# Performance work log

Hardware: AMD Instinct MI355X
Metric: run time of the kernel (lower is better)

The kernel has to match this reference:

```python
import jax, jax.numpy as jnp
import numpy as np

T, B, F = 160, 640, 40
HID, PROJ, LAYERS = 768, 256, 3


def lstm_proj_layer(x, Wk, b, Wp, reverse=False):
    # x: [T, B, in]; Wk: [in+PROJ, 4*HID]; b: [4*HID]; Wp: [HID, PROJ]
    nb = x.shape[1]
    c0 = jnp.zeros((nb, HID), x.dtype)
    h0 = jnp.zeros((nb, PROJ), x.dtype)

    def step(carry, xt):
        c, h = carry
        z = jnp.concatenate([xt, h], axis=-1) @ Wk + b
        i, j, f, o = jnp.split(z, 4, axis=-1)  # TF LSTMCell gate order i,j,f,o
        c = jax.nn.sigmoid(f + 1.0) * c + jax.nn.sigmoid(i) * jnp.tanh(j)  # forget_bias=1.0
        h = (jax.nn.sigmoid(o) * jnp.tanh(c)) @ Wp  # projection
        return (c, h), h

    _, ys = jax.lax.scan(step, (c0, h0), x, reverse=reverse)
    return ys  # [T, B, PROJ], time-aligned with input even when reverse=True


def _run_stack(x, params, reverse):
    for (Wk, b, Wp) in params:
        x = lstm_proj_layer(x, Wk, b, Wp, reverse=reverse)
    return x


def setup_inputs() -> dict:
    key = jax.random.key(0)
    keys = jax.random.split(key, 1 + 6 * LAYERS)
    inp = {"batch": jax.random.normal(keys[0], (T, B, F), dtype=jnp.float32)}
    ki = 1
    for d in ("fw", "bw"):
        for l in range(LAYERS):
            in_dim = F if l == 0 else PROJ
            inp[f"Wk_{d}{l}"] = jax.random.normal(keys[ki], (in_dim + PROJ, 4 * HID), dtype=jnp.float32) * 0.05
            inp[f"b_{d}{l}"] = jnp.zeros((4 * HID,), dtype=jnp.float32)
            inp[f"Wp_{d}{l}"] = jax.random.normal(keys[ki + 1], (HID, PROJ), dtype=jnp.float32) * 0.05
            ki += 2
    return inp


def reference(batch,
              Wk_fw0, b_fw0, Wp_fw0, Wk_fw1, b_fw1, Wp_fw1, Wk_fw2, b_fw2, Wp_fw2,
              Wk_bw0, b_bw0, Wp_bw0, Wk_bw1, b_bw1, Wp_bw1, Wk_bw2, b_bw2, Wp_bw2):
    fw_params = [(Wk_fw0, b_fw0, Wp_fw0), (Wk_fw1, b_fw1, Wp_fw1), (Wk_fw2, b_fw2, Wp_fw2)]
    bw_params = [(Wk_bw0, b_bw0, Wp_bw0), (Wk_bw1, b_bw1, Wp_bw1), (Wk_bw2, b_bw2, Wp_bw2)]
    out_fw = _run_stack(batch, fw_params, reverse=False)
    out_bw = _run_stack(batch, bw_params, reverse=True)
    outputs = jnp.concatenate([out_fw, out_bw], axis=2)  # [T, B, 2*PROJ]
    embedded = (outputs[0] + outputs[-1]) / 2.0
    # tf.nn.l2_normalize semantics
    embedded = embedded * jax.lax.rsqrt(jnp.maximum(jnp.sum(embedded * embedded, axis=-1, keepdims=True), 1e-12))
    return embedded
```

## Files before the change

### kernel.cpp

```cpp
#include <hip/hip_runtime.h>


typedef _Float16 h8 __attribute__((ext_vector_type(8)));
typedef float f4 __attribute__((ext_vector_type(4)));

#define T_STEPS 160
#define NB 640
#define HID 768
#define PROJ 256
#define NGATE 3072

__device__ __forceinline__ float sigm(float x) { return 1.0f / (1.0f + __expf(-x)); }
__device__ __forceinline__ float tanh_fast(float x) { return 2.0f / (1.0f + __expf(-2.0f * x)) - 1.0f; }

struct GateArgs {
  const _Float16* A0[6];
  const _Float16* A1[6];
  const _Float16* Bw[6];
  const float*    bias[6];
  float*          cst[6];
  _Float16*       g[6];
  int w0[6];
  int lda0[6];
  int K[6];
  int act[6];
};

struct ProjArgs {
  const _Float16* G[6];
  const _Float16* Wp[6];
  _Float16* out[6];
  _Float16* out2[6];
  int act[6];
};

__global__ __launch_bounds__(256, 3) void gate_step(GateArgs args) {
  const int z = blockIdx.z;
  if (!args.act[z]) return;

  __shared__ __align__(16) char sm[36864];
  _Float16 (*As)[72] = (_Float16(*)[72])sm;
  _Float16 (*Bs)[72] = (_Float16(*)[72])(sm + 18432);
  float (*zs)[65] = (float(*)[65])sm;

  const _Float16* A0 = args.A0[z];
  const _Float16* A1 = args.A1[z];
  const _Float16* Bw = args.Bw[z];
  const int w0 = args.w0[z], lda0 = args.lda0[z], K = args.K[z];
  const int n0 = blockIdx.x * 128;
  const int m0 = blockIdx.y * 128;
  const int tid = threadIdx.x;
  const int lane = tid & 63;
  const int wv = tid >> 6;
  const int wm = (wv & 1) * 64;
  const int wn = (wv >> 1) * 64;

  f4 acc[4][4] = {};

  const int lr = tid >> 3;
  const int lkg = (tid & 7) * 8;

  for (int k0 = 0; k0 < K; k0 += 64) {
    const int gk = k0 + lkg;
    h8 av[4], bv[4];
    if (gk < w0) {
#pragma unroll
      for (int r = 0; r < 4; ++r)
        av[r] = *(const h8*)(A0 + (size_t)(m0 + lr + 32 * r) * lda0 + gk);
    } else {
#pragma unroll
      for (int r = 0; r < 4; ++r)
        av[r] = *(const h8*)(A1 + (size_t)(m0 + lr + 32 * r) * 256 + (gk - w0));
    }
#pragma unroll
    for (int r = 0; r < 4; ++r)
      bv[r] = *(const h8*)(Bw + (size_t)(n0 + lr + 32 * r) * K + gk);
    __syncthreads();
#pragma unroll
    for (int r = 0; r < 4; ++r) {
      *(h8*)&As[lr + 32 * r][lkg] = av[r];
      *(h8*)&Bs[lr + 32 * r][lkg] = bv[r];
    }
    __syncthreads();
#pragma unroll
    for (int kk = 0; kk < 2; ++kk) {
      const int kq = ((lane >> 4) * 8) + kk * 32;
      h8 bf[4];
#pragma unroll
      for (int j = 0; j < 4; ++j)
        bf[j] = *(const h8*)&Bs[wn + (lane & 15) + 16 * j][kq];
#pragma unroll
      for (int i = 0; i < 4; ++i) {
        h8 af = *(const h8*)&As[wm + (lane & 15) + 16 * i][kq];
#pragma unroll
        for (int j = 0; j < 4; ++j)
          acc[i][j] = __builtin_amdgcn_mfma_f32_16x16x32_f16(af, bf[j], acc[i][j], 0, 0, 0);
      }
    }
  }

  const float* bias = args.bias[z];
  float* cstate = args.cst[z];
  _Float16* gout = args.g[z];
#pragma unroll
  for (int p = 0; p < 2; ++p) {
    __syncthreads();
    if ((wv >> 1) == p) {
#pragma unroll
      for (int mi = 0; mi < 4; ++mi)
#pragma unroll
        for (int ni = 0; ni < 4; ++ni)
#pragma unroll
          for (int r = 0; r < 4; ++r) {
            int row = wm + mi * 16 + ((lane >> 4) << 2) + r;
            int col = ni * 16 + (lane & 15);
            zs[row][col] = acc[mi][ni][r];
          }
    }
    __syncthreads();
    const int u0 = (n0 + p * 64) >> 2;
#pragma unroll
    for (int it = 0; it < 8; ++it) {
      int item = it * 256 + tid;
      int row = item >> 4;
      int u = item & 15;
      float zi = zs[row][4 * u + 0] + bias[0 * HID + u0 + u];
      float zj = zs[row][4 * u + 1] + bias[1 * HID + u0 + u];
      float zf = zs[row][4 * u + 2] + bias[2 * HID + u0 + u];
      float zo = zs[row][4 * u + 3] + bias[3 * HID + u0 + u];
      size_t co = (size_t)(m0 + row) * HID + u0 + u;
      float cold = cstate[co];
      float cnew = sigm(zf + 1.0f) * cold + sigm(zi) * tanh_fast(zj);
      float g = sigm(zo) * tanh_fast(cnew);
      cstate[co] = cnew;
      gout[co] = (_Float16)g;
    }
  }
}

__global__ __launch_bounds__(256) void proj_step(ProjArgs args) {
  const int z = blockIdx.z;
  if (!args.act[z]) return;

  __shared__ __align__(16) _Float16 As[64][72];
  __shared__ __align__(16) _Float16 Bs[64][72];

  const _Float16* A = args.G[z];
  const _Float16* B = args.Wp[z];
  const int n0 = blockIdx.x * 64;
  const int m0 = blockIdx.y * 64;
  const int tid = threadIdx.x;
  const int lane = tid & 63;
  const int wv = tid >> 6;
  const int wm = (wv & 1) * 32;
  const int wn = (wv >> 1) * 32;

  f4 acc[2][2] = {};
  const int lr = tid >> 3;
  const int lkg = (tid & 7) * 8;

  for (int k0 = 0; k0 < HID; k0 += 64) {
    const int gk = k0 + lkg;
    h8 av0 = *(const h8*)(A + (size_t)(m0 + lr) * HID + gk);
    h8 av1 = *(const h8*)(A + (size_t)(m0 + lr + 32) * HID + gk);
    h8 bv0 = *(const h8*)(B + (size_t)(n0 + lr) * HID + gk);
    h8 bv1 = *(const h8*)(B + (size_t)(n0 + lr + 32) * HID + gk);
    __syncthreads();
    *(h8*)&As[lr][lkg] = av0;
    *(h8*)&As[lr + 32][lkg] = av1;
    *(h8*)&Bs[lr][lkg] = bv0;
    *(h8*)&Bs[lr + 32][lkg] = bv1;
    __syncthreads();
    const int mr = wm + (lane & 15);
    const int nr = wn + (lane & 15);
#pragma unroll
    for (int kk = 0; kk < 2; ++kk) {
      const int kq = ((lane >> 4) * 8) + kk * 32;
      h8 a0 = *(const h8*)&As[mr][kq];
      h8 a1 = *(const h8*)&As[mr + 16][kq];
      h8 b0 = *(const h8*)&Bs[nr][kq];
      h8 b1 = *(const h8*)&Bs[nr + 16][kq];
      acc[0][0] = __builtin_amdgcn_mfma_f32_16x16x32_f16(a0, b0, acc[0][0], 0, 0, 0);
      acc[0][1] = __builtin_amdgcn_mfma_f32_16x16x32_f16(a0, b1, acc[0][1], 0, 0, 0);
      acc[1][0] = __builtin_amdgcn_mfma_f32_16x16x32_f16(a1, b0, acc[1][0], 0, 0, 0);
      acc[1][1] = __builtin_amdgcn_mfma_f32_16x16x32_f16(a1, b1, acc[1][1], 0, 0, 0);
    }
  }

  _Float16* outp = args.out[z];
  _Float16* out2 = args.out2[z];
#pragma unroll
  for (int mi = 0; mi < 2; ++mi)
#pragma unroll
    for (int ni = 0; ni < 2; ++ni)
#pragma unroll
      for (int r = 0; r < 4; ++r) {
        int row = wm + mi * 16 + ((lane >> 4) << 2) + r;
        int col = wn + ni * 16 + (lane & 15);
        _Float16 v = (_Float16)acc[mi][ni][r];
        size_t o = (size_t)(m0 + row) * PROJ + (n0 + col);
        outp[o] = v;
        if (out2) out2[o] = v;
      }
}

__global__ void convX(const float* __restrict__ X, _Float16* __restrict__ X16, size_t total) {
  size_t i = (size_t)blockIdx.x * 256 + threadIdx.x;
  if (i >= total) return;
  int p = (int)(i & 63);
  size_t tb = i >> 6;
  float v = (p < 40) ? X[tb * 40 + p] : 0.0f;
  X16[i] = (_Float16)v;
}

__global__ void conv_wk(const float* __restrict__ Wk, _Float16* __restrict__ out,
                        int mode, int Kpad, size_t total) {
  size_t i = (size_t)blockIdx.x * 256 + threadIdx.x;
  if (i >= total) return;
  int k = (int)(i % Kpad);
  int n = (int)(i / Kpad);
  int u = n >> 2, g = n & 3;
  int col = g * HID + u;
  float v;
  if (mode == 0) {
    if (k < 40)      v = Wk[(size_t)k * NGATE + col];
    else if (k < 64) v = 0.0f;
    else             v = Wk[(size_t)(k - 24) * NGATE + col];
  } else {
    v = Wk[(size_t)k * NGATE + col];
  }
  out[i] = (_Float16)v;
}

__global__ void conv_wp(const float* __restrict__ Wp, _Float16* __restrict__ out, size_t total) {
  size_t i = (size_t)blockIdx.x * 256 + threadIdx.x;
  if (i >= total) return;
  int k = (int)(i % HID);
  int c = (int)(i / HID);
  out[i] = (_Float16)Wp[(size_t)k * PROJ + c];
}

__global__ __launch_bounds__(256) void readout(const _Float16* __restrict__ E, float* __restrict__ out) {
  const size_t SL = (size_t)NB * PROJ;
  int b = blockIdx.x, tid = threadIdx.x;
  float v[2];
  float ss = 0.0f;
#pragma unroll
  for (int i = 0; i < 2; ++i) {
    int j = tid + i * 256;
    int d = j >> 8, c = j & 255;
    const _Float16* base = E + (size_t)d * 2 * SL;
    float a = (float)base[(size_t)b * PROJ + c];
    float zv = (float)base[SL + (size_t)b * PROJ + c];
    v[i] = 0.5f * (a + zv);
    ss += v[i] * v[i];
  }
#pragma unroll
  for (int off = 32; off; off >>= 1) ss += __shfl_down(ss, off);
  __shared__ float ps[4];
  if ((tid & 63) == 0) ps[tid >> 6] = ss;
  __syncthreads();
  float tot = ps[0] + ps[1] + ps[2] + ps[3];
  float nrm = rsqrtf(fmaxf(tot, 1e-12f));
  out[(size_t)b * 512 + tid] = v[0] * nrm;
  out[(size_t)b * 512 + tid + 256] = v[1] * nrm;
}

extern "C" void kernel_launch(void* const* d_in, const int* in_sizes, int n_in,
                              void* d_out, int out_size, void* d_ws, size_t ws_size,
                              hipStream_t stream) {
  (void)in_sizes; (void)n_in; (void)out_size; (void)ws_size;
  const float* X = (const float*)d_in[0];
  const float* Wk[2][3]; const float* Bi[2][3]; const float* Wp[2][3];
  for (int d = 0; d < 2; ++d)
    for (int l = 0; l < 3; ++l) {
      int base = 1 + d * 9 + l * 3;
      Wk[d][l] = (const float*)d_in[base];
      Bi[d][l] = (const float*)d_in[base + 1];
      Wp[d][l] = (const float*)d_in[base + 2];
    }

  char* ws = (char*)d_ws;
  size_t off = 0;
  auto alloc = [&](size_t bytes) -> void* {
    void* p = ws + off;
    off += (bytes + 255) & ~(size_t)255;
    return p;
  };

  const size_t SL = (size_t)NB * PROJ;

  _Float16* X16 = (_Float16*)alloc((size_t)T_STEPS * NB * 64 * 2);
  _Float16* WkT[2][3];
  for (int d = 0; d < 2; ++d)
    for (int l = 0; l < 3; ++l)
      WkT[d][l] = (_Float16*)alloc((size_t)NGATE * (l == 0 ? 320 : 512) * 2);
  _Float16* WpT[2][3];
  for (int d = 0; d < 2; ++d)
    for (int l = 0; l < 3; ++l)
      WpT[d][l] = (_Float16*)alloc((size_t)PROJ * HID * 2);
  _Float16* Hbuf = (_Float16*)alloc(6UL * 4 * SL * 2);
  float* cst = (float*)alloc(6UL * NB * HID * 4);
  _Float16* gbuf = (_Float16*)alloc(6UL * NB * HID * 2);
  _Float16* embed = (_Float16*)alloc(4UL * SL * 2);

  auto Hslot = [&](int l, int d, int slot) -> _Float16* {
    return Hbuf + (((size_t)(l * 2 + d) * 4) + slot) * SL;
  };

  {
    size_t tot = (size_t)T_STEPS * NB * 64;
    convX<<<dim3((unsigned)((tot + 255) / 256)), 256, 0, stream>>>(X, X16, tot);
  }
  for (int d = 0; d < 2; ++d)
    for (int l = 0; l < 3; ++l) {
      int Kpad = (l == 0) ? 320 : 512;
      size_t tot = (size_t)NGATE * Kpad;
      conv_wk<<<dim3((unsigned)((tot + 255) / 256)), 256, 0, stream>>>(
          Wk[d][l], WkT[d][l], (l == 0) ? 0 : 1, Kpad, tot);
      size_t totp = (size_t)PROJ * HID;
      conv_wp<<<dim3((unsigned)((totp + 255) / 256)), 256, 0, stream>>>(Wp[d][l], WpT[d][l], totp);
    }
  hipMemsetAsync(Hbuf, 0, 6UL * 4 * SL * 2, stream);
  hipMemsetAsync(cst, 0, 6UL * NB * HID * 4, stream);

  for (int s = 0; s <= 161; ++s) {
    GateArgs ga{};
    ProjArgs pa{};
    for (int l = 0; l < 3; ++l)
      for (int d = 0; d < 2; ++d) {
        int z = l * 2 + d;
        int t = s - l;
        if (t < 0 || t > 159) { ga.act[z] = 0; pa.act[z] = 0; continue; }
        int tt = (d == 0) ? t : 159 - t;
        ga.act[z] = 1; pa.act[z] = 1;
        if (l == 0) {
          ga.A0[z] = X16 + (size_t)tt * NB * 64;
          ga.w0[z] = 64; ga.lda0[z] = 64; ga.K[z] = 320;
        } else {
          ga.A0[z] = Hslot(l - 1, d, (tt + 1) & 3);
          ga.w0[z] = 256; ga.lda0[z] = 256; ga.K[z] = 512;
        }
        int rdslot = (d == 0) ? (tt & 3) : ((tt + 2) & 3);
        ga.A1[z] = Hslot(l, d, rdslot);
        ga.Bw[z] = WkT[d][l];
        ga.bias[z] = Bi[d][l];
        ga.cst[z] = cst + (size_t)z * NB * HID;
        ga.g[z] = gbuf + (size_t)z * NB * HID;

        pa.G[z] = gbuf + (size_t)z * NB * HID;
        pa.Wp[z] = WpT[d][l];
        pa.out[z] = Hslot(l, d, (tt + 1) & 3);
        pa.out2[z] = nullptr;
        if (l == 2 && (tt == 0 || tt == 159))
          pa.out2[z] = embed + ((size_t)d * 2 + (tt == 0 ? 0 : 1)) * SL;
      }
    gate_step<<<dim3(24, 5, 6), 256, 0, stream>>>(ga);
    proj_step<<<dim3(4, 10, 6), 256, 0, stream>>>(pa);
  }

  readout<<<dim3(NB), 256, 0, stream>>>(embed, (float*)d_out);
}
```

Before: 5.876 ms.

## Fuse gate and projection kernels per step with atomic flag handoff

Merges the per-step gate GEMM kernel and the projection GEMM kernel into a single launch of 960 blocks. Projection blocks spin on per-row-tile atomic counters that the gate blocks increment with release semantics once they finish, so projection of a row tile can start as soon as its gate tiles are done, with no kernel boundary in between. This halves the number of launches and allows gate and projection work to overlap. The risk is that the spin-waiting projection blocks could occupy CUs while gate blocks are still unscheduled, which would cost throughput or deadlock, though lower block indices are typically dispatched first.

```diff
diff --git a/kernel.cpp b/kernel.cpp
--- a/kernel.cpp
+++ b/kernel.cpp
@@ -13,7 +13,7 @@
 __device__ __forceinline__ float sigm(float x) { return 1.0f / (1.0f + __expf(-x)); }
 __device__ __forceinline__ float tanh_fast(float x) { return 2.0f / (1.0f + __expf(-2.0f * x)) - 1.0f; }
 
-struct GateArgs {
+struct FusedArgs {
   const _Float16* A0[6];
   const _Float16* A1[6];
   const _Float16* Bw[6];
@@ -24,21 +24,14 @@
   int lda0[6];
   int K[6];
   int act[6];
-};
-
-struct ProjArgs {
-  const _Float16* G[6];
   const _Float16* Wp[6];
   _Float16* out[6];
   _Float16* out2[6];
-  int act[6];
+  int* flags;
+  int thresh[6];
 };
 
-__global__ __launch_bounds__(256, 3) void gate_step(GateArgs args) {
-  const int z = blockIdx.z;
-  if (!args.act[z]) return;
-
-  __shared__ __align__(16) char sm[36864];
+__device__ __forceinline__ void gate_body(const FusedArgs& args, char* sm, int z, int bx, int by) {
   _Float16 (*As)[72] = (_Float16(*)[72])sm;
   _Float16 (*Bs)[72] = (_Float16(*)[72])(sm + 18432);
   float (*zs)[65] = (float(*)[65])sm;
@@ -47,8 +40,8 @@
   const _Float16* A1 = args.A1[z];
   const _Float16* Bw = args.Bw[z];
   const int w0 = args.w0[z], lda0 = args.lda0[z], K = args.K[z];
-  const int n0 = blockIdx.x * 128;
-  const int m0 = blockIdx.y * 128;
+  const int n0 = bx * 128;
+  const int m0 = by * 128;
   const int tid = threadIdx.x;
   const int lane = tid & 63;
   const int wv = tid >> 6;
@@ -136,19 +129,30 @@
       gout[co] = (_Float16)g;
     }
   }
-}
-
-__global__ __launch_bounds__(256) void proj_step(ProjArgs args) {
-  const int z = blockIdx.z;
-  if (!args.act[z]) return;
-
-  __shared__ __align__(16) _Float16 As[64][72];
-  __shared__ __align__(16) _Float16 Bs[64][72];
-
-  const _Float16* A = args.G[z];
+
+  __syncthreads();
+  if (tid == 0)
+    __hip_atomic_fetch_add(&args.flags[(z * 5 + by) * 32], 1,
+                           __ATOMIC_RELEASE, __HIP_MEMORY_SCOPE_AGENT);
+}
+
+__device__ __forceinline__ void proj_body(const FusedArgs& args, char* sm, int z, int bx, int by) {
+  _Float16 (*As)[72] = (_Float16(*)[72])sm;
+  _Float16 (*Bs)[72] = (_Float16(*)[72])(sm + 9216);
+
+  if (threadIdx.x == 0) {
+    int* f = &args.flags[(z * 5 + (by >> 1)) * 32];
+    const int th = args.thresh[z];
+    while (__hip_atomic_load(f, __ATOMIC_RELAXED, __HIP_MEMORY_SCOPE_AGENT) < th)
+      __builtin_amdgcn_s_sleep(2);
+    (void)__hip_atomic_load(f, __ATOMIC_ACQUIRE, __HIP_MEMORY_SCOPE_AGENT);
+  }
+  __syncthreads();
+
+  const _Float16* A = args.g[z];
   const _Float16* B = args.Wp[z];
-  const int n0 = blockIdx.x * 64;
-  const int m0 = blockIdx.y * 64;
+  const int n0 = bx * 64;
+  const int m0 = by * 64;
   const int tid = threadIdx.x;
   const int lane = tid & 63;
   const int wv = tid >> 6;
@@ -202,6 +206,21 @@
         outp[o] = v;
         if (out2) out2[o] = v;
       }
+}
+
+__global__ __launch_bounds__(256, 3) void fused_step(FusedArgs args) {
+  __shared__ __align__(16) char sm[36864];
+  const int b = blockIdx.x;
+  if (b < 720) {
+    const int z = b / 120, rem = b % 120;
+    if (!args.act[z]) return;
+    gate_body(args, sm, z, rem % 24, rem / 24);
+  } else {
+    const int p = b - 720;
+    const int z = p / 40, rem = p % 40;
+    if (!args.act[z]) return;
+    proj_body(args, sm, z, rem % 4, rem / 4);
+  }
 }
 
 __global__ void convX(const float* __restrict__ X, _Float16* __restrict__ X16, size_t total) {
@@ -303,6 +322,7 @@
   float* cst = (float*)alloc(6UL * NB * HID * 4);
   _Float16* gbuf = (_Float16*)alloc(6UL * NB * HID * 2);
   _Float16* embed = (_Float16*)alloc(4UL * SL * 2);
+  int* flags = (int*)alloc(30UL * 32 * 4);
 
   auto Hslot = [&](int l, int d, int slot) -> _Float16* {
     return Hbuf + (((size_t)(l * 2 + d) * 4) + slot) * SL;
@@ -323,40 +343,42 @@
     }
   hipMemsetAsync(Hbuf, 0, 6UL * 4 * SL * 2, stream);
   hipMemsetAsync(cst, 0, 6UL * NB * HID * 4, stream);
-
+  hipMemsetAsync(flags, 0, 30UL * 32 * 4, stream);
+
+  int actcnt[6] = {0, 0, 0, 0, 0, 0};
   for (int s = 0; s <= 161; ++s) {
-    GateArgs ga{};
-    ProjArgs pa{};
+    FusedArgs fa{};
+    fa.flags = flags;
     for (int l = 0; l < 3; ++l)
       for (int d = 0; d < 2; ++d) {
         int z = l * 2 + d;
         int t = s - l;
-        if (t < 0 || t > 159) { ga.act[z] = 0; pa.act[z] = 0; continue; }
+        if (t < 0 || t > 159) { fa.act[z] = 0; continue; }
         int tt = (d == 0) ? t : 159 - t;
-        ga.act[z] = 1; pa.act[z] = 1;
+        fa.act[z] = 1;
+        actcnt[z]++;
+        fa.thresh[z] = 24 * actcnt[z];
         if (l == 0) {
-          ga.A0[z] = X16 + (size_t)tt * NB * 64;
-          ga.w0[z] = 64; ga.lda0[z] = 64; ga.K[z] = 320;
+          fa.A0[z] = X16 + (size_t)tt * NB * 64;
+          fa.w0[z] = 64; fa.lda0[z] = 64; fa.K[z] = 320;
         } else {
-          ga.A0[z] = Hslot(l - 1, d, (tt + 1) & 3);
-          ga.w0[z] = 256; ga.lda0[z] = 256; ga.K[z] = 512;
+          fa.A0[z] = Hslot(l - 1, d, (tt + 1) & 3);
+          fa.w0[z] = 256; fa.lda0[z] = 256; fa.K[z] = 512;
         }
         int rdslot = (d == 0) ? (tt & 3) : ((tt + 2) & 3);
-        ga.A1[z] = Hslot(l, d, rdslot);
-        ga.Bw[z] = WkT[d][l];
-        ga.bias[z] = Bi[d][l];
-        ga.cst[z] = cst + (size_t)z * NB * HID;
-        ga.g[z] = gbuf + (size_t)z * NB * HID;
-
-        pa.G[z] = gbuf + (size_t)z * NB * HID;
-        pa.Wp[z] = WpT[d][l];
-        pa.out[z] = Hslot(l, d, (tt + 1) & 3);
-        pa.out2[z] = nullptr;
+        fa.A1[z] = Hslot(l, d, rdslot);
+        fa.Bw[z] = WkT[d][l];
+        fa.bias[z] = Bi[d][l];
+        fa.cst[z] = cst + (size_t)z * NB * HID;
+        fa.g[z] = gbuf + (size_t)z * NB * HID;
+
+        fa.Wp[z] = WpT[d][l];
+        fa.out[z] = Hslot(l, d, (tt + 1) & 3);
+        fa.out2[z] = nullptr;
         if (l == 2 && (tt == 0 || tt == 159))
-          pa.out2[z] = embed + ((size_t)d * 2 + (tt == 0 ? 0 : 1)) * SL;
+          fa.out2[z] = embed + ((size_t)d * 2 + (tt == 0 ? 0 : 1)) * SL;
       }
-    gate_step<<<dim3(24, 5, 6), 256, 0, stream>>>(ga);
-    proj_step<<<dim3(4, 10, 6), 256, 0, stream>>>(pa);
+    fused_step<<<dim3(960), 256, 0, stream>>>(fa);
   }
 
   readout<<<dim3(NB), 256, 0, stream>>>(embed, (float*)d_out);
```

Measured after the change: 9.381 ms. +59.6%, slower.

## Pre-swizzle weights into MFMA fragment layout and load B directly to registers

Applied to the files above, without the earlier changes.

Weight conversion kernels now write Wk and Wp in a tiled layout matching the MFMA operand fragment order, so each lane reads its B fragment with one contiguous 16-byte global load. The B shared-memory staging and its LDS traffic are removed from both the gate and projection GEMMs. The A tile is also register-prefetched one k-step ahead to overlap global loads with MFMA work. Each wave now fetches its own B fragments from global/L2 instead of sharing them through LDS, which adds duplicate global reads across waves that share a column tile.

```diff
diff --git a/kernel.cpp b/kernel.cpp
--- a/kernel.cpp
+++ b/kernel.cpp
@@ -40,13 +40,13 @@
 
   __shared__ __align__(16) char sm[36864];
   _Float16 (*As)[72] = (_Float16(*)[72])sm;
-  _Float16 (*Bs)[72] = (_Float16(*)[72])(sm + 18432);
   float (*zs)[65] = (float(*)[65])sm;
 
   const _Float16* A0 = args.A0[z];
   const _Float16* A1 = args.A1[z];
   const _Float16* Bw = args.Bw[z];
   const int w0 = args.w0[z], lda0 = args.lda0[z], K = args.K[z];
+  const int KI = K >> 6;
   const int n0 = blockIdx.x * 128;
   const int m0 = blockIdx.y * 128;
   const int tid = threadIdx.x;
@@ -54,15 +54,16 @@
   const int wv = tid >> 6;
   const int wm = (wv & 1) * 64;
   const int wn = (wv >> 1) * 64;
+  const int ntb = (n0 + wn) >> 4;
 
   f4 acc[4][4] = {};
 
   const int lr = tid >> 3;
   const int lkg = (tid & 7) * 8;
 
-  for (int k0 = 0; k0 < K; k0 += 64) {
-    const int gk = k0 + lkg;
-    h8 av[4], bv[4];
+  h8 av[4];
+  {
+    const int gk = lkg;
     if (gk < w0) {
 #pragma unroll
       for (int r = 0; r < 4; ++r)
@@ -72,29 +73,53 @@
       for (int r = 0; r < 4; ++r)
         av[r] = *(const h8*)(A1 + (size_t)(m0 + lr + 32 * r) * 256 + (gk - w0));
     }
+  }
+
+  for (int k0 = 0, ki = 0; k0 < K; k0 += 64, ++ki) {
+    h8 bf0[4];
+#pragma unroll
+    for (int j = 0; j < 4; ++j) {
+      const _Float16* u = Bw + (((size_t)(ntb + j) * KI + ki) << 10) + lane * 8;
+      bf0[j] = *(const h8*)u;
+    }
+    __syncthreads();
 #pragma unroll
     for (int r = 0; r < 4; ++r)
-      bv[r] = *(const h8*)(Bw + (size_t)(n0 + lr + 32 * r) * K + gk);
-    __syncthreads();
-#pragma unroll
-    for (int r = 0; r < 4; ++r) {
       *(h8*)&As[lr + 32 * r][lkg] = av[r];
-      *(h8*)&Bs[lr + 32 * r][lkg] = bv[r];
-    }
-    __syncthreads();
-#pragma unroll
-    for (int kk = 0; kk < 2; ++kk) {
-      const int kq = ((lane >> 4) * 8) + kk * 32;
-      h8 bf[4];
-#pragma unroll
-      for (int j = 0; j < 4; ++j)
-        bf[j] = *(const h8*)&Bs[wn + (lane & 15) + 16 * j][kq];
+    if (k0 + 64 < K) {
+      const int gk = k0 + 64 + lkg;
+      if (gk < w0) {
+#pragma unroll
+        for (int r = 0; r < 4; ++r)
+          av[r] = *(const h8*)(A0 + (size_t)(m0 + lr + 32 * r) * lda0 + gk);
+      } else {
+#pragma unroll
+        for (int r = 0; r < 4; ++r)
+          av[r] = *(const h8*)(A1 + (size_t)(m0 + lr + 32 * r) * 256 + (gk - w0));
+      }
+    }
+    __syncthreads();
+    h8 bf1[4];
+#pragma unroll
+    for (int j = 0; j < 4; ++j) {
+      const _Float16* u = Bw + (((size_t)(ntb + j) * KI + ki) << 10) + lane * 8;
+      bf1[j] = *(const h8*)(u + 512);
+    }
+    {
+      const int kq0 = (lane >> 4) * 8;
 #pragma unroll
       for (int i = 0; i < 4; ++i) {
-        h8 af = *(const h8*)&As[wm + (lane & 15) + 16 * i][kq];
+        h8 af = *(const h8*)&As[wm + (lane & 15) + 16 * i][kq0];
 #pragma unroll
         for (int j = 0; j < 4; ++j)
-          acc[i][j] = __builtin_amdgcn_mfma_f32_16x16x32_f16(af, bf[j], acc[i][j], 0, 0, 0);
+          acc[i][j] = __builtin_amdgcn_mfma_f32_16x16x32_f16(af, bf0[j], acc[i][j], 0, 0, 0);
+      }
+#pragma unroll
+      for (int i = 0; i < 4; ++i) {
+        h8 af = *(const h8*)&As[wm + (lane & 15) + 16 * i][kq0 + 32];
+#pragma unroll
+        for (int j = 0; j < 4; ++j)
+          acc[i][j] = __builtin_amdgcn_mfma_f32_16x16x32_f16(af, bf1[j], acc[i][j], 0, 0, 0);
       }
     }
   }
@@ -143,7 +168,6 @@
   if (!args.act[z]) return;
 
   __shared__ __align__(16) _Float16 As[64][72];
-  __shared__ __align__(16) _Float16 Bs[64][72];
 
   const _Float16* A = args.G[z];
   const _Float16* B = args.Wp[z];
@@ -154,36 +178,52 @@
   const int wv = tid >> 6;
   const int wm = (wv & 1) * 32;
   const int wn = (wv >> 1) * 32;
+  const int ntb = (n0 + wn) >> 4;
 
   f4 acc[2][2] = {};
   const int lr = tid >> 3;
   const int lkg = (tid & 7) * 8;
 
-  for (int k0 = 0; k0 < HID; k0 += 64) {
-    const int gk = k0 + lkg;
-    h8 av0 = *(const h8*)(A + (size_t)(m0 + lr) * HID + gk);
-    h8 av1 = *(const h8*)(A + (size_t)(m0 + lr + 32) * HID + gk);
-    h8 bv0 = *(const h8*)(B + (size_t)(n0 + lr) * HID + gk);
-    h8 bv1 = *(const h8*)(B + (size_t)(n0 + lr + 32) * HID + gk);
+  h8 av0 = *(const h8*)(A + (size_t)(m0 + lr) * HID + lkg);
+  h8 av1 = *(const h8*)(A + (size_t)(m0 + lr + 32) * HID + lkg);
+
+  for (int k0 = 0, ki = 0; k0 < HID; k0 += 64, ++ki) {
+    h8 bf0[2];
+#pragma unroll
+    for (int j = 0; j < 2; ++j) {
+      const _Float16* u = B + (((size_t)(ntb + j) * 12 + ki) << 10) + lane * 8;
+      bf0[j] = *(const h8*)u;
+    }
     __syncthreads();
     *(h8*)&As[lr][lkg] = av0;
     *(h8*)&As[lr + 32][lkg] = av1;
-    *(h8*)&Bs[lr][lkg] = bv0;
-    *(h8*)&Bs[lr + 32][lkg] = bv1;
-    __syncthreads();
+    if (k0 + 64 < HID) {
+      const int gk = k0 + 64 + lkg;
+      av0 = *(const h8*)(A + (size_t)(m0 + lr) * HID + gk);
+      av1 = *(const h8*)(A + (size_t)(m0 + lr + 32) * HID + gk);
+    }
+    __syncthreads();
+    h8 bf1[2];
+#pragma unroll
+    for (int j = 0; j < 2; ++j) {
+      const _Float16* u = B + (((size_t)(ntb + j) * 12 + ki) << 10) + lane * 8;
+      bf1[j] = *(const h8*)(u + 512);
+    }
     const int mr = wm + (lane & 15);
-    const int nr = wn + (lane & 15);
-#pragma unroll
-    for (int kk = 0; kk < 2; ++kk) {
-      const int kq = ((lane >> 4) * 8) + kk * 32;
-      h8 a0 = *(const h8*)&As[mr][kq];
-      h8 a1 = *(const h8*)&As[mr + 16][kq];
-      h8 b0 = *(const h8*)&Bs[nr][kq];
-      h8 b1 = *(const h8*)&Bs[nr + 16][kq];
-      acc[0][0] = __builtin_amdgcn_mfma_f32_16x16x32_f16(a0, b0, acc[0][0], 0, 0, 0);
-      acc[0][1] = __builtin_amdgcn_mfma_f32_16x16x32_f16(a0, b1, acc[0][1], 0, 0, 0);
-      acc[1][0] = __builtin_amdgcn_mfma_f32_16x16x32_f16(a1, b0, acc[1][0], 0, 0, 0);
-      acc[1][1] = __builtin_amdgcn_mfma_f32_16x16x32_f16(a1, b1, acc[1][1], 0, 0, 0);
+    {
+      const int kq0 = (lane >> 4) * 8;
+      h8 a0 = *(const h8*)&As[mr][kq0];
+      h8 a1 = *(const h8*)&As[mr + 16][kq0];
+      acc[0][0] = __builtin_amdgcn_mfma_f32_16x16x32_f16(a0, bf0[0], acc[0][0], 0, 0, 0);
+      acc[0][1] = __builtin_amdgcn_mfma_f32_16x16x32_f16(a0, bf0[1], acc[0][1], 0, 0, 0);
+      acc[1][0] = __builtin_amdgcn_mfma_f32_16x16x32_f16(a1, bf0[0], acc[1][0], 0, 0, 0);
+      acc[1][1] = __builtin_amdgcn_mfma_f32_16x16x32_f16(a1, bf0[1], acc[1][1], 0, 0, 0);
+      h8 a2 = *(const h8*)&As[mr][kq0 + 32];
+      h8 a3 = *(const h8*)&As[mr + 16][kq0 + 32];
+      acc[0][0] = __builtin_amdgcn_mfma_f32_16x16x32_f16(a2, bf1[0], acc[0][0], 0, 0, 0);
+      acc[0][1] = __builtin_amdgcn_mfma_f32_16x16x32_f16(a2, bf1[1], acc[0][1], 0, 0, 0);
+      acc[1][0] = __builtin_amdgcn_mfma_f32_16x16x32_f16(a3, bf1[0], acc[1][0], 0, 0, 0);
+      acc[1][1] = __builtin_amdgcn_mfma_f32_16x16x32_f16(a3, bf1[1], acc[1][1], 0, 0, 0);
     }
   }
 
@@ -229,7 +269,12 @@
   } else {
     v = Wk[(size_t)k * NGATE + col];
   }
-  out[i] = (_Float16)v;
+  const int KI = Kpad >> 6;
+  size_t addr = (((size_t)(n >> 4) * KI + (k >> 6)) << 10)
+              + (size_t)((k >> 5) & 1) * 512
+              + (size_t)((((k >> 3) & 3) * 16 + (n & 15)) * 8)
+              + (size_t)(k & 7);
+  out[addr] = (_Float16)v;
 }
 
 __global__ void conv_wp(const float* __restrict__ Wp, _Float16* __restrict__ out, size_t total) {
@@ -237,7 +282,12 @@
   if (i >= total) return;
   int k = (int)(i % HID);
   int c = (int)(i / HID);
-  out[i] = (_Float16)Wp[(size_t)k * PROJ + c];
+  float v = Wp[(size_t)k * PROJ + c];
+  size_t addr = (((size_t)(c >> 4) * 12 + (k >> 6)) << 10)
+              + (size_t)((k >> 5) & 1) * 512
+              + (size_t)((((k >> 3) & 3) * 16 + (c & 15)) * 8)
+              + (size_t)(k & 7);
+  out[addr] = (_Float16)v;
 }
 
 __global__ __launch_bounds__(256) void readout(const _Float16* __restrict__ E, float* __restrict__ out) {
```

New measurement: 5.637 ms. 1.04x faster.

## Pre-swizzle weights into MFMA fragment layout and drop LDS staging in GEMMs

Applied to the files above, without the earlier changes.

Weight conversion kernels now write Wk and Wp in a tiled layout that matches the MFMA B-fragment order, so each lane loads its fragment with one contiguous 16-byte global load. The gate and projection GEMMs drop LDS staging and both __syncthreads per K-step: B fragments come straight from the swizzled weights and A fragments straight from global memory. This removes barrier and LDS traffic. In exchange, A rows are loaded redundantly by waves that share them, and the A loads are strided rather than coalesced through shared memory.

```diff
diff --git a/kernel.cpp b/kernel.cpp
--- a/kernel.cpp
+++ b/kernel.cpp
@@ -38,15 +38,13 @@
   const int z = blockIdx.z;
   if (!args.act[z]) return;
 
-  __shared__ __align__(16) char sm[36864];
-  _Float16 (*As)[72] = (_Float16(*)[72])sm;
-  _Float16 (*Bs)[72] = (_Float16(*)[72])(sm + 18432);
-  float (*zs)[65] = (float(*)[65])sm;
+  __shared__ __align__(16) float zs[128][65];
 
   const _Float16* A0 = args.A0[z];
   const _Float16* A1 = args.A1[z];
   const _Float16* Bw = args.Bw[z];
   const int w0 = args.w0[z], lda0 = args.lda0[z], K = args.K[z];
+  const int KI = K >> 6;
   const int n0 = blockIdx.x * 128;
   const int m0 = blockIdx.y * 128;
   const int tid = threadIdx.x;
@@ -54,44 +52,31 @@
   const int wv = tid >> 6;
   const int wm = (wv & 1) * 64;
   const int wn = (wv >> 1) * 64;
+  const int ntb = (n0 + wn) >> 4;
+  const int fr = lane & 15;
+  const int fk = (lane >> 4) * 8;
 
   f4 acc[4][4] = {};
 
-  const int lr = tid >> 3;
-  const int lkg = (tid & 7) * 8;
-
-  for (int k0 = 0; k0 < K; k0 += 64) {
-    const int gk = k0 + lkg;
-    h8 av[4], bv[4];
-    if (gk < w0) {
-#pragma unroll
-      for (int r = 0; r < 4; ++r)
-        av[r] = *(const h8*)(A0 + (size_t)(m0 + lr + 32 * r) * lda0 + gk);
-    } else {
-#pragma unroll
-      for (int r = 0; r < 4; ++r)
-        av[r] = *(const h8*)(A1 + (size_t)(m0 + lr + 32 * r) * 256 + (gk - w0));
-    }
-#pragma unroll
-    for (int r = 0; r < 4; ++r)
-      bv[r] = *(const h8*)(Bw + (size_t)(n0 + lr + 32 * r) * K + gk);
-    __syncthreads();
-#pragma unroll
-    for (int r = 0; r < 4; ++r) {
-      *(h8*)&As[lr + 32 * r][lkg] = av[r];
-      *(h8*)&Bs[lr + 32 * r][lkg] = bv[r];
-    }
-    __syncthreads();
+  for (int ki = 0; ki < KI; ++ki) {
+    h8 bf0[4], bf1[4];
+#pragma unroll
+    for (int j = 0; j < 4; ++j) {
+      const _Float16* u = Bw + (((size_t)(ntb + j) * KI + ki) << 10) + lane * 8;
+      bf0[j] = *(const h8*)u;
+      bf1[j] = *(const h8*)(u + 512);
+    }
 #pragma unroll
     for (int kk = 0; kk < 2; ++kk) {
-      const int kq = ((lane >> 4) * 8) + kk * 32;
-      h8 bf[4];
-#pragma unroll
-      for (int j = 0; j < 4; ++j)
-        bf[j] = *(const h8*)&Bs[wn + (lane & 15) + 16 * j][kq];
+      const int gk = ki * 64 + kk * 32 + fk;
+      const _Float16* Ab;
+      int lda;
+      if (gk < w0) { Ab = A0 + gk; lda = lda0; }
+      else         { Ab = A1 + (gk - w0); lda = 256; }
+      const h8* bf = kk ? bf1 : bf0;
 #pragma unroll
       for (int i = 0; i < 4; ++i) {
-        h8 af = *(const h8*)&As[wm + (lane & 15) + 16 * i][kq];
+        h8 af = *(const h8*)(Ab + (size_t)(m0 + wm + fr + 16 * i) * lda);
 #pragma unroll
         for (int j = 0; j < 4; ++j)
           acc[i][j] = __builtin_amdgcn_mfma_f32_16x16x32_f16(af, bf[j], acc[i][j], 0, 0, 0);
@@ -142,9 +127,6 @@
   const int z = blockIdx.z;
   if (!args.act[z]) return;
 
-  __shared__ __align__(16) _Float16 As[64][72];
-  __shared__ __align__(16) _Float16 Bs[64][72];
-
   const _Float16* A = args.G[z];
   const _Float16* B = args.Wp[z];
   const int n0 = blockIdx.x * 64;
@@ -154,36 +136,30 @@
   const int wv = tid >> 6;
   const int wm = (wv & 1) * 32;
   const int wn = (wv >> 1) * 32;
+  const int ntb = (n0 + wn) >> 4;
+  const int fr = lane & 15;
+  const int fk = (lane >> 4) * 8;
 
   f4 acc[2][2] = {};
-  const int lr = tid >> 3;
-  const int lkg = (tid & 7) * 8;
-
-  for (int k0 = 0; k0 < HID; k0 += 64) {
-    const int gk = k0 + lkg;
-    h8 av0 = *(const h8*)(A + (size_t)(m0 + lr) * HID + gk);
-    h8 av1 = *(const h8*)(A + (size_t)(m0 + lr + 32) * HID + gk);
-    h8 bv0 = *(const h8*)(B + (size_t)(n0 + lr) * HID + gk);
-    h8 bv1 = *(const h8*)(B + (size_t)(n0 + lr + 32) * HID + gk);
-    __syncthreads();
-    *(h8*)&As[lr][lkg] = av0;
-    *(h8*)&As[lr + 32][lkg] = av1;
-    *(h8*)&Bs[lr][lkg] = bv0;
-    *(h8*)&Bs[lr + 32][lkg] = bv1;
-    __syncthreads();
-    const int mr = wm + (lane & 15);
-    const int nr = wn + (lane & 15);
+
+  for (int ki = 0; ki < 12; ++ki) {
+    h8 bf0[2], bf1[2];
+#pragma unroll
+    for (int j = 0; j < 2; ++j) {
+      const _Float16* u = B + (((size_t)(ntb + j) * 12 + ki) << 10) + lane * 8;
+      bf0[j] = *(const h8*)u;
+      bf1[j] = *(const h8*)(u + 512);
+    }
 #pragma unroll
     for (int kk = 0; kk < 2; ++kk) {
-      const int kq = ((lane >> 4) * 8) + kk * 32;
-      h8 a0 = *(const h8*)&As[mr][kq];
-      h8 a1 = *(const h8*)&As[mr + 16][kq];
-      h8 b0 = *(const h8*)&Bs[nr][kq];
-      h8 b1 = *(const h8*)&Bs[nr + 16][kq];
-      acc[0][0] = __builtin_amdgcn_mfma_f32_16x16x32_f16(a0, b0, acc[0][0], 0, 0, 0);
-      acc[0][1] = __builtin_amdgcn_mfma_f32_16x16x32_f16(a0, b1, acc[0][1], 0, 0, 0);
-      acc[1][0] = __builtin_amdgcn_mfma_f32_16x16x32_f16(a1, b0, acc[1][0], 0, 0, 0);
-      acc[1][1] = __builtin_amdgcn_mfma_f32_16x16x32_f16(a1, b1, acc[1][1], 0, 0, 0);
+      const int gk = ki * 64 + kk * 32 + fk;
+      const h8* bf = kk ? bf1 : bf0;
+#pragma unroll
+      for (int mi = 0; mi < 2; ++mi) {
+        h8 af = *(const h8*)(A + (size_t)(m0 + wm + fr + 16 * mi) * HID + gk);
+        acc[mi][0] = __builtin_amdgcn_mfma_f32_16x16x32_f16(af, bf[0], acc[mi][0], 0, 0, 0);
+        acc[mi][1] = __builtin_amdgcn_mfma_f32_16x16x32_f16(af, bf[1], acc[mi][1], 0, 0, 0);
+      }
     }
   }
 
@@ -229,7 +205,12 @@
   } else {
     v = Wk[(size_t)k * NGATE + col];
   }
-  out[i] = (_Float16)v;
+  const int KI = Kpad >> 6;
+  size_t addr = (((size_t)(n >> 4) * KI + (k >> 6)) << 10)
+              + (size_t)((k >> 5) & 1) * 512
+              + (size_t)((((k >> 3) & 3) * 16 + (n & 15)) * 8)
+              + (size_t)(k & 7);
+  out[addr] = (_Float16)v;
 }
 
 __global__ void conv_wp(const float* __restrict__ Wp, _Float16* __restrict__ out, size_t total) {
@@ -237,7 +218,12 @@
   if (i >= total) return;
   int k = (int)(i % HID);
   int c = (int)(i / HID);
-  out[i] = (_Float16)Wp[(size_t)k * PROJ + c];
+  float v = Wp[(size_t)k * PROJ + c];
+  size_t addr = (((size_t)(c >> 4) * 12 + (k >> 6)) << 10)
+              + (size_t)((k >> 5) & 1) * 512
+              + (size_t)((((k >> 3) & 3) * 16 + (c & 15)) * 8)
+              + (size_t)(k & 7);
+  out[addr] = (_Float16)v;
 }
 
 __global__ __launch_bounds__(256) void readout(const _Float16* __restrict__ E, float* __restrict__ out) {
```

After: 8.940 ms. +52.1%, slower.
